# Kernel tuning notes

Hardware: AMD Instinct MI355X
Metric: run time of the kernel (lower is better)

Reference implementation:

```python
import jax, jax.numpy as jnp
import numpy as np

B, S, D = 1, 2048, 6144
H, KV, HD = 48, 8, 128  # query heads, kv heads, head dim
THETA = 10000.0


def _rope_tables(seq_len, head_dim, theta):
    pos = jnp.arange(seq_len, dtype=jnp.float32)
    inv_freq = 1.0 / (theta ** (jnp.arange(0, head_dim, 2, dtype=jnp.float32) / head_dim))
    freqs = pos[:, None] * inv_freq[None, :]                 # [S, HD/2]
    emb = jnp.concatenate([freqs, freqs], axis=-1)           # [S, HD]
    return jnp.cos(emb), jnp.sin(emb)


def setup_inputs() -> dict:
    key = jax.random.key(0)
    k1, k2, k3 = jax.random.split(key, 3)
    hidden_states = jax.random.normal(k1, (B, S, D), dtype=jnp.float32) * 0.02
    w_qkv = jax.random.normal(k2, (D, (H + 2 * KV) * HD), dtype=jnp.float32) * 0.02
    w_out = jax.random.normal(k3, (H * HD, D), dtype=jnp.float32) * 0.02
    cos, sin = _rope_tables(S, HD, THETA)
    return {"hidden_states": hidden_states, "cos": cos, "sin": sin,
            "w_qkv": w_qkv, "w_out": w_out}


def _rotate_half(x):
    x1, x2 = jnp.split(x, 2, axis=-1)
    return jnp.concatenate([-x2, x1], axis=-1)


def reference(hidden_states, cos, sin, w_qkv, w_out):
    b, s, d = hidden_states.shape
    # fused QKV projection
    qkv = jnp.einsum('bsd,de->bse', hidden_states, w_qkv)
    q = qkv[..., : H * HD].reshape(b, s, H, HD)
    k = qkv[..., H * HD: (H + KV) * HD].reshape(b, s, KV, HD)
    v = qkv[..., (H + KV) * HD:].reshape(b, s, KV, HD)
    # rotary embedding (rotate-half form)
    c = cos[None, :, None, :]
    sn = sin[None, :, None, :]
    q = q * c + _rotate_half(q) * sn
    k = k * c + _rotate_half(k) * sn
    # GQA: expand kv heads to query heads
    rep = H // KV
    k = jnp.repeat(k, rep, axis=2)  # [b, s, H, HD]
    v = jnp.repeat(v, rep, axis=2)
    scale = 1.0 / jnp.sqrt(jnp.float32(HD))
    scores = jnp.einsum('bqhd,bkhd->bhqk', q, k) * scale     # [b,H,S,S]
    causal = jnp.tril(jnp.ones((s, s), dtype=bool))
    scores = jnp.where(causal[None, None], scores, jnp.float32(-1e30))
    attn = jax.nn.softmax(scores, axis=-1)
    out = jnp.einsum('bhqk,bkhd->bqhd', attn, v).reshape(b, s, H * HD)
    return jnp.einsum('bsd,de->bse', out, w_out)
```

## Files before the change

### kernel.cpp

```cpp
#include <hip/hip_runtime.h>


#define S_   2048
#define D_   6144
#define H_   48
#define KV_  8
#define HD_  128
#define NQK  8192
#define REP  6

typedef __attribute__((ext_vector_type(8)))  __bf16 bf16x8;
typedef __attribute__((ext_vector_type(4)))  __bf16 bf16x4;
typedef __attribute__((ext_vector_type(2)))  __bf16 bf16x2;
typedef __attribute__((ext_vector_type(4)))  float  f32x4;
typedef __attribute__((ext_vector_type(16))) float  f32x16;
typedef __attribute__((ext_vector_type(4)))  float  float4v;

__device__ __forceinline__ void gl_lds16(const void* g, void* l) {
  __builtin_amdgcn_global_load_lds(
      (const __attribute__((address_space(1))) void*)g,
      (__attribute__((address_space(3))) void*)l, 16, 0, 0);
}

__device__ __forceinline__ unsigned pack2(float a, float b) {
  union { bf16x2 v; unsigned u; } x;
  x.v[0] = (__bf16)a; x.v[1] = (__bf16)b;
  return x.u;
}

__global__ __launch_bounds__(256) void cvt_bf16(const float* __restrict__ in,
                                                __bf16* __restrict__ out, int n4) {
  int stride = gridDim.x * 256;
  for (int i = blockIdx.x * 256 + threadIdx.x; i < n4; i += stride) {
    float4v v = ((const float4v*)in)[i];
    bf16x4 o;
    o[0] = (__bf16)v[0]; o[1] = (__bf16)v[1];
    o[2] = (__bf16)v[2]; o[3] = (__bf16)v[3];
    ((bf16x4*)out)[i] = o;
  }
}

__global__ __launch_bounds__(256) void wtrans(const float* __restrict__ src,
                                              __bf16* __restrict__ dst,
                                              int K, int N) {
  __shared__ float t[32][33];
  const int n0 = blockIdx.x * 32, k0 = blockIdx.y * 32;
  const int tx = threadIdx.x, ty = threadIdx.y;
#pragma unroll
  for (int r = 0; r < 4; ++r)
    t[ty + r * 8][tx] = src[(size_t)(k0 + ty + r * 8) * N + n0 + tx];
  __syncthreads();
#pragma unroll
  for (int r = 0; r < 4; ++r)
    dst[(size_t)(n0 + ty + r * 8) * K + k0 + tx] = (__bf16)t[tx][ty + r * 8];
}

template <typename CT, int BN>
__global__ __launch_bounds__(512, 2) void gemm_bt(const __bf16* __restrict__ A,
                                                  const __bf16* __restrict__ BT,
                                                  CT* __restrict__ C,
                                                  int M, int N, int K) {
  constexpr int NB = BN / 64;
  constexpr int NF = BN / 64;
  __shared__ __align__(16) __bf16 As[2][256 * 64];
  __shared__ __align__(16) __bf16 Bs[2][BN * 64];
  const int tid = threadIdx.x;
  const int w = tid >> 6, l = tid & 63;
  const int lr = l & 15, lg = l >> 4;
  const int wm = w >> 2, wn = w & 3;
  const int nwg = gridDim.x * gridDim.y;
  int bid = blockIdx.y * gridDim.x + blockIdx.x;
  bid = (bid & 7) * (nwg >> 3) + (bid >> 3);
  const int m0 = (bid / gridDim.x) * 256, n0 = (bid % gridDim.x) * BN;
  const int nkt = K >> 6;

  auto sA = [&](int T, int half) {
    const int buf = T & 1, k0 = T << 6;
#pragma unroll
    for (int jj = 0; jj < 2; ++jj) {
      int j = half * 2 + jj;
      int idx = j * 512 + tid;
      int row = idx >> 3;
      int c = (idx & 7) ^ (row & 7);
      gl_lds16(A + (size_t)(m0 + row) * K + k0 + c * 8,
               As[buf] + (size_t)(j * 512 + w * 64) * 8);
    }
  };
  auto sB = [&](int T) {
    const int buf = T & 1, k0 = T << 6;
#pragma unroll
    for (int j = 0; j < NB; ++j) {
      int idx = j * 512 + tid;
      int row = idx >> 3;
      int c = (idx & 7) ^ (row & 7);
      gl_lds16(BT + (size_t)(n0 + row) * K + k0 + c * 8,
               Bs[buf] + (size_t)(j * 512 + w * 64) * 8);
    }
  };
  auto rdA = [&](const __bf16* Ab, int mh, int kk, bf16x8* afr) {
#pragma unroll
    for (int m = 0; m < 4; ++m) {
      int row = wm * 128 + (mh * 4 + m) * 16 + lr;
      afr[m] = *(const bf16x8*)(Ab + (size_t)row * 64
                                + (((kk * 4 + lg) ^ (lr & 7)) * 8));
    }
  };
  auto rdB = [&](const __bf16* Bb, int kk, bf16x8* bfr) {
#pragma unroll
    for (int n = 0; n < NF; ++n) {
      int row = wn * (BN / 4) + n * 16 + lr;
      bfr[n] = *(const bf16x8*)(Bb + (size_t)row * 64
                                + (((kk * 4 + lg) ^ (lr & 7)) * 8));
    }
  };
#define LGKM0 asm volatile("s_waitcnt lgkmcnt(0)" ::: "memory")
#define SBAR  __builtin_amdgcn_s_barrier()
#define SCHB  __builtin_amdgcn_sched_barrier(0)
#define MFMA_CLUSTER(ACC_OFF)                                                   \
  __builtin_amdgcn_s_setprio(1);                                               \
  _Pragma("unroll")                                                             \
  for (int m = 0; m < 4; ++m)                                                   \
    _Pragma("unroll")                                                           \
    for (int n = 0; n < NF; ++n)                                                \
      acc[(ACC_OFF) + m][n] = __builtin_amdgcn_mfma_f32_16x16x32_bf16(          \
          afr[m], bfr[n], acc[(ACC_OFF) + m][n], 0, 0, 0);                      \
  __builtin_amdgcn_s_setprio(0)

  f32x4 acc[8][NF] = {};
  sA(0, 0); sA(0, 1); sB(0);

  for (int T = 0; T < nkt; ++T) {
    const __bf16* Ab = As[T & 1];
    const __bf16* Bb = Bs[T & 1];
    bf16x8 afr[4], bfr[NF];
    if (T + 1 < nkt) {
      sA(T + 1, 0);
      asm volatile("s_waitcnt vmcnt(2)" ::: "memory");
    } else {
      asm volatile("s_waitcnt vmcnt(0)" ::: "memory");
    }
    SBAR;
    rdA(Ab, 0, 0, afr);
    rdB(Bb, 0, bfr);
    LGKM0; SCHB;
    MFMA_CLUSTER(0);
    rdA(Ab, 1, 0, afr);
    LGKM0;
    if (T + 1 < nkt) sA(T + 1, 1);
    SBAR; SCHB;
    MFMA_CLUSTER(4);
    rdA(Ab, 0, 1, afr);
    rdB(Bb, 1, bfr);
    LGKM0;
    if (T + 1 < nkt) sB(T + 1);
    SBAR; SCHB;
    MFMA_CLUSTER(0);
    rdA(Ab, 1, 1, afr);
    LGKM0;
    SBAR; SCHB;
    MFMA_CLUSTER(4);
  }
#undef LGKM0
#undef SBAR
#undef SCHB
#undef MFMA_CLUSTER
#pragma unroll
  for (int m = 0; m < 8; ++m)
#pragma unroll
    for (int n = 0; n < NF; ++n)
#pragma unroll
      for (int j = 0; j < 4; ++j) {
        int row = m0 + wm * 128 + m * 16 + lg * 4 + j;
        int col = n0 + wn * (BN / 4) + n * 16 + lr;
        C[(size_t)row * N + col] = (CT)acc[m][n][j];
      }
}

__global__ __launch_bounds__(256) void rope_qk(const __bf16* __restrict__ qkv,
                                               const float* __restrict__ cosT,
                                               const float* __restrict__ sinT,
                                               __bf16* __restrict__ Qo,
                                               __bf16* __restrict__ Ko) {
  const int s = blockIdx.x;
  const __bf16* base = qkv + (size_t)s * NQK;
  const float* ct = cosT + s * HD_;
  const float* st = sinT + s * HD_;
  const float scale = 0.1275174313f;
  for (int q4 = threadIdx.x; q4 < H_ * HD_ / 4; q4 += 256) {
    int h = q4 >> 5, d = (q4 & 31) * 4;
    bf16x4 x  = *(const bf16x4*)(base + h * HD_ + d);
    bf16x4 xr = (d < 64) ? *(const bf16x4*)(base + h * HD_ + d + 64)
                         : *(const bf16x4*)(base + h * HD_ + d - 64);
    float4v c4 = *(const float4v*)(ct + d);
    float4v s4 = *(const float4v*)(st + d);
    bf16x4 o;
#pragma unroll
    for (int j = 0; j < 4; ++j) {
      float r = (d < 64) ? -(float)xr[j] : (float)xr[j];
      o[j] = (__bf16)(((float)x[j] * c4[j] + r * s4[j]) * scale);
    }
    *(bf16x4*)(Qo + ((size_t)s * H_ + h) * HD_ + d) = o;
  }
  for (int q4 = threadIdx.x; q4 < KV_ * HD_ / 4; q4 += 256) {
    int h = q4 >> 5, d = (q4 & 31) * 4;
    const __bf16* kb = base + H_ * HD_;
    bf16x4 x  = *(const bf16x4*)(kb + h * HD_ + d);
    bf16x4 xr = (d < 64) ? *(const bf16x4*)(kb + h * HD_ + d + 64)
                         : *(const bf16x4*)(kb + h * HD_ + d - 64);
    float4v c4 = *(const float4v*)(ct + d);
    float4v s4 = *(const float4v*)(st + d);
    bf16x4 o;
#pragma unroll
    for (int j = 0; j < 4; ++j) {
      float r = (d < 64) ? -(float)xr[j] : (float)xr[j];
      o[j] = (__bf16)((float)x[j] * c4[j] + r * s4[j]);
    }
    *(bf16x4*)(Ko + ((size_t)s * KV_ + h) * HD_ + d) = o;
  }
}

__global__ __launch_bounds__(256) void v_trans(const __bf16* __restrict__ qkv,
                                               __bf16* __restrict__ Vt) {
  __shared__ __bf16 t[32][36];
  const int s0 = blockIdx.x * 32, d0 = blockIdx.y * 32, h = blockIdx.z;
  const int tx = threadIdx.x, ty = threadIdx.y;
  *(bf16x4*)&t[ty][tx * 4] =
      *(const bf16x4*)(qkv + (size_t)(s0 + ty) * NQK + (H_ + KV_) * HD_ + h * HD_ + d0 + tx * 4);
  __syncthreads();
  bf16x4 o;
#pragma unroll
  for (int j = 0; j < 4; ++j) o[j] = t[tx * 4 + j][ty];
  *(bf16x4*)(Vt + ((size_t)h * HD_ + d0 + ty) * S_ + s0 + tx * 4) = o;
}

__global__ __launch_bounds__(256, 2) void attn(const __bf16* __restrict__ Q,
                                               const __bf16* __restrict__ Kb,
                                               const __bf16* __restrict__ Vt,
                                               __bf16* __restrict__ O) {
  __shared__ __align__(16) __bf16 Ks[2][64 * 128];
  __shared__ __align__(16) __bf16 Vs[2][128 * 64];
  const int bx = blockIdx.x, h = blockIdx.y, kvh = h / REP;
  const int tid = threadIdx.x, w = tid >> 6, l = tid & 63;
  const int c = l & 31, g = l >> 5;
  const int qb = bx * 128;
  const int qrow = qb + w * 32 + c;
  const int tmax_w = (qb + w * 32 + 31) >> 6;
  const int NT = (qb >> 6) + 2;

  auto stage = [&](int t) {
    const int buf = t & 1;
    const int kbase = t << 6;
#pragma unroll
    for (int j = 0; j < 4; ++j) {
      int idx = j * 256 + tid;
      int row = idx >> 4, cc = (idx & 15) ^ (row & 15);
      gl_lds16(Kb + ((size_t)(kbase + row) * KV_ + kvh) * HD_ + cc * 8,
               Ks[buf] + (size_t)(j * 256 + w * 64) * 8);
    }
#pragma unroll
    for (int j = 0; j < 4; ++j) {
      int idx = j * 256 + tid;
      int row = idx >> 3, cc = (idx & 7) ^ (row & 7);
      gl_lds16(Vt + (size_t)(kvh * HD_ + row) * S_ + kbase + cc * 8,
               Vs[buf] + (size_t)(j * 256 + w * 64) * 8);
    }
  };

  bf16x8 qf[8];
  const __bf16* qp = Q + ((size_t)qrow * H_ + h) * HD_ + g * 8;
#pragma unroll
  for (int st = 0; st < 8; ++st) qf[st] = *(const bf16x8*)(qp + st * 16);

  f32x16 o[4] = {};
  float m = -1e30f, lsum = 0.f;

  stage(0);
  __syncthreads();
  for (int t = 0; t < NT; ++t) {
    const int buf = t & 1;
    if (t + 1 < NT) stage(t + 1);
    if (t <= tmax_w) {
      const int kbase = t << 6;
      f32x16 s0 = {}, s1 = {};
      __builtin_amdgcn_s_setprio(1);
#pragma unroll
      for (int st = 0; st < 8; ++st) {
        int ch = ((st * 2 + g) ^ (c & 15)) * 8;
        bf16x8 k0 = *(const bf16x8*)(Ks[buf] + (size_t)c * 128 + ch);
        bf16x8 k1 = *(const bf16x8*)(Ks[buf] + (size_t)(32 + c) * 128 + ch);
        s0 = __builtin_amdgcn_mfma_f32_32x32x16_bf16(k0, qf[st], s0, 0, 0, 0);
        s1 = __builtin_amdgcn_mfma_f32_32x32x16_bf16(k1, qf[st], s1, 0, 0, 0);
      }
      __builtin_amdgcn_s_setprio(0);
      if (t == tmax_w) {
#pragma unroll
        for (int r = 0; r < 16; ++r) {
          int krow = (r & 3) + 8 * (r >> 2) + 4 * g;
          if (kbase + krow > qrow)      s0[r] = -1e30f;
          if (kbase + 32 + krow > qrow) s1[r] = -1e30f;
        }
      }
      float mj = s0[0];
#pragma unroll
      for (int r = 1; r < 16; ++r) mj = fmaxf(mj, s0[r]);
#pragma unroll
      for (int r = 0; r < 16; ++r) mj = fmaxf(mj, s1[r]);
      mj = fmaxf(mj, __shfl_xor(mj, 32));
      float mnew = fmaxf(m, mj);
      float sc = __builtin_amdgcn_exp2f(m - mnew);
      float rs = 0.f;
      float p0[16], p1[16];
#pragma unroll
      for (int r = 0; r < 16; ++r) { p0[r] = __builtin_amdgcn_exp2f(s0[r] - mnew); rs += p0[r]; }
#pragma unroll
      for (int r = 0; r < 16; ++r) { p1[r] = __builtin_amdgcn_exp2f(s1[r] - mnew); rs += p1[r]; }
      rs += __shfl_xor(rs, 32);
      lsum = lsum * sc + rs;
      m = mnew;
#pragma unroll
      for (int db = 0; db < 4; ++db)
#pragma unroll
        for (int r = 0; r < 16; ++r) o[db][r] *= sc;
      unsigned bq[4][4];
#pragma unroll
      for (int n = 0; n < 2; ++n)
#pragma unroll
        for (int tq = 0; tq < 2; ++tq) {
          const float* pp = n ? p1 : p0;
          unsigned q0 = pack2(pp[8 * tq + 0], pp[8 * tq + 1]);
          unsigned q1 = pack2(pp[8 * tq + 2], pp[8 * tq + 3]);
          unsigned q2 = pack2(pp[8 * tq + 4], pp[8 * tq + 5]);
          unsigned q3 = pack2(pp[8 * tq + 6], pp[8 * tq + 7]);
          unsigned v0 = g ? q0 : q2;
          unsigned v1 = g ? q1 : q3;
          unsigned sh0 = (unsigned)__shfl_xor((int)v0, 32);
          unsigned sh1 = (unsigned)__shfl_xor((int)v1, 32);
          int s = n * 2 + tq;
          bq[s][0] = g ? sh0 : q0;
          bq[s][1] = g ? sh1 : q1;
          bq[s][2] = g ? q2 : sh0;
          bq[s][3] = g ? q3 : sh1;
        }
      __builtin_amdgcn_s_setprio(1);
#pragma unroll
      for (int s = 0; s < 4; ++s) {
        union { unsigned u[4]; bf16x8 v; } bb;
        bb.u[0] = bq[s][0]; bb.u[1] = bq[s][1]; bb.u[2] = bq[s][2]; bb.u[3] = bq[s][3];
#pragma unroll
        for (int db = 0; db < 4; ++db) {
          int ch = ((s * 2 + g) ^ (c & 7)) * 8;
          bf16x8 vfr = *(const bf16x8*)(Vs[buf] + (size_t)(db * 32 + c) * 64 + ch);
          o[db] = __builtin_amdgcn_mfma_f32_32x32x16_bf16(vfr, bb.v, o[db], 0, 0, 0);
        }
      }
      __builtin_amdgcn_s_setprio(0);
    }
    if (t + 1 < NT) __syncthreads();
  }
  float inv = 1.f / lsum;
#pragma unroll
  for (int db = 0; db < 4; ++db)
#pragma unroll
    for (int rg = 0; rg < 4; ++rg) {
      bf16x4 ov;
#pragma unroll
      for (int j = 0; j < 4; ++j) ov[j] = (__bf16)(o[db][rg * 4 + j] * inv);
      *(bf16x4*)(O + (size_t)qrow * D_ + h * HD_ + db * 32 + rg * 8 + g * 4) = ov;
    }
}

extern "C" void kernel_launch(void* const* d_in, const int* in_sizes, int n_in,
                              void* d_out, int out_size, void* d_ws, size_t ws_size,
                              hipStream_t stream) {
  const float* hidden = (const float*)d_in[0];
  const float* cosT   = (const float*)d_in[1];
  const float* sinT   = (const float*)d_in[2];
  const float* w_qkv  = (const float*)d_in[3];
  const float* w_out  = (const float*)d_in[4];
  float* out = (float*)d_out;
  char* ws = (char*)d_ws;

  __bf16* wT   = (__bf16*)ws;
  __bf16* hb   = (__bf16*)(ws + 100663296);
  __bf16* qkvb = (__bf16*)(ws + 100663296 + 25165824);
  __bf16* q_b  = (__bf16*)(ws + 100663296 + 25165824 + 33554432);
  __bf16* k_b  = q_b + (size_t)S_ * H_ * HD_;
  __bf16* vt_b = k_b + (size_t)S_ * KV_ * HD_;

  cvt_bf16<<<dim3(2048), dim3(256), 0, stream>>>(hidden, hb, (int)((size_t)S_ * D_ / 4));
  wtrans<<<dim3(NQK / 32, D_ / 32), dim3(32, 8), 0, stream>>>(w_qkv, wT, D_, NQK);
  gemm_bt<__bf16, 256><<<dim3(NQK / 256, S_ / 256), dim3(512), 0, stream>>>(hb, wT, qkvb, S_, NQK, D_);
  rope_qk<<<dim3(S_), dim3(256), 0, stream>>>(qkvb, cosT, sinT, q_b, k_b);
  v_trans<<<dim3(S_ / 32, HD_ / 32, KV_), dim3(8, 32), 0, stream>>>(qkvb, vt_b);
  wtrans<<<dim3(D_ / 32, D_ / 32), dim3(32, 8), 0, stream>>>(w_out, wT, D_, D_);
  attn<<<dim3(S_ / 128, H_), dim3(256), 0, stream>>>(q_b, k_b, vt_b, hb);
  gemm_bt<float, 192><<<dim3(D_ / 192, S_ / 256), dim3(512), 0, stream>>>(hb, wT, out, S_, D_, D_);
}
```

Measured before the change: 687.8 us.

## Issue all next-tile loads upfront in GEMM and drop fine-grained waits

The GEMM main loop now stages the whole next K-tile (A and B) in one batch right after the first fragment reads, and waits for vmcnt(0) only at the end of each iteration. It drops the split A/B staging, the per-cluster lgkmcnt waits and the sched_barriers, so the compiler can schedule LDS reads and MFMAs more freely. The cost is that asynchronous global-to-LDS writes into the other buffer now overlap the whole iteration. The explicit LDS-read waits are gone, so ordering relies on the compiler's waitcnt insertion, and the schedule control given by the sched_barriers is lost.

```diff
diff --git a/kernel.cpp b/kernel.cpp
--- a/kernel.cpp
+++ b/kernel.cpp
@@ -74,20 +74,16 @@
   const int m0 = (bid / gridDim.x) * 256, n0 = (bid % gridDim.x) * BN;
   const int nkt = K >> 6;
 
-  auto sA = [&](int T, int half) {
+  auto stage_all = [&](int T) {
     const int buf = T & 1, k0 = T << 6;
 #pragma unroll
-    for (int jj = 0; jj < 2; ++jj) {
-      int j = half * 2 + jj;
+    for (int j = 0; j < 4; ++j) {
       int idx = j * 512 + tid;
       int row = idx >> 3;
       int c = (idx & 7) ^ (row & 7);
       gl_lds16(A + (size_t)(m0 + row) * K + k0 + c * 8,
                As[buf] + (size_t)(j * 512 + w * 64) * 8);
     }
-  };
-  auto sB = [&](int T) {
-    const int buf = T & 1, k0 = T << 6;
 #pragma unroll
     for (int j = 0; j < NB; ++j) {
       int idx = j * 512 + tid;
@@ -113,9 +109,7 @@
                                 + (((kk * 4 + lg) ^ (lr & 7)) * 8));
     }
   };
-#define LGKM0 asm volatile("s_waitcnt lgkmcnt(0)" ::: "memory")
 #define SBAR  __builtin_amdgcn_s_barrier()
-#define SCHB  __builtin_amdgcn_sched_barrier(0)
 #define MFMA_CLUSTER(ACC_OFF)                                                   \
   __builtin_amdgcn_s_setprio(1);                                               \
   _Pragma("unroll")                                                             \
@@ -127,42 +121,33 @@
   __builtin_amdgcn_s_setprio(0)
 
   f32x4 acc[8][NF] = {};
-  sA(0, 0); sA(0, 1); sB(0);
+  stage_all(0);
+  asm volatile("s_waitcnt vmcnt(0)" ::: "memory");
+  SBAR;
 
   for (int T = 0; T < nkt; ++T) {
     const __bf16* Ab = As[T & 1];
     const __bf16* Bb = Bs[T & 1];
     bf16x8 afr[4], bfr[NF];
-    if (T + 1 < nkt) {
-      sA(T + 1, 0);
-      asm volatile("s_waitcnt vmcnt(2)" ::: "memory");
-    } else {
-      asm volatile("s_waitcnt vmcnt(0)" ::: "memory");
-    }
-    SBAR;
     rdA(Ab, 0, 0, afr);
     rdB(Bb, 0, bfr);
-    LGKM0; SCHB;
+    if (T + 1 < nkt) stage_all(T + 1);
     MFMA_CLUSTER(0);
+    SBAR;
     rdA(Ab, 1, 0, afr);
-    LGKM0;
-    if (T + 1 < nkt) sA(T + 1, 1);
-    SBAR; SCHB;
     MFMA_CLUSTER(4);
+    SBAR;
     rdA(Ab, 0, 1, afr);
     rdB(Bb, 1, bfr);
-    LGKM0;
-    if (T + 1 < nkt) sB(T + 1);
-    SBAR; SCHB;
     MFMA_CLUSTER(0);
+    SBAR;
     rdA(Ab, 1, 1, afr);
-    LGKM0;
-    SBAR; SCHB;
     MFMA_CLUSTER(4);
-  }
-#undef LGKM0
+    asm volatile("s_waitcnt lgkmcnt(0)" ::: "memory");
+    if (T + 1 < nkt) asm volatile("s_waitcnt vmcnt(0)" ::: "memory");
+    SBAR;
+  }
 #undef SBAR
-#undef SCHB
 #undef MFMA_CLUSTER
 #pragma unroll
   for (int m = 0; m < 8; ++m)
```

Result: faster. 662.2 us (-3.7%).
